# Performance work log

Measured on AMD Instinct MI355X. Metric: run time of the kernel, lower is better.

Reference implementation:

```python
import jax, jax.numpy as jnp
import numpy as np

B, C, F, T, D = 8, 128, 256, 128, 32


def setup_inputs() -> dict:
    key = jax.random.key(0)
    ks = jax.random.split(key, 7)
    x = jax.random.normal(ks[0], (B, C, F, T), jnp.float32)
    # 1x1 Conv2d over the T axis == linear map on T; weights [out, T], bias [out]
    Wk = jax.random.normal(ks[1], (D, T), jnp.float32) * 0.05
    bk = jax.random.normal(ks[2], (D,), jnp.float32) * 0.05
    Wq = jax.random.normal(ks[3], (D, T), jnp.float32) * 0.05
    bq = jax.random.normal(ks[4], (D,), jnp.float32) * 0.05
    Wv = jax.random.normal(ks[5], (T, T), jnp.float32) * 0.05
    bv = jax.random.normal(ks[6], (T,), jnp.float32) * 0.05
    return {"x": x, "Wk": Wk, "bk": bk, "Wq": Wq, "bq": bq, "Wv": Wv, "bv": bv}


def _proj(xp, W, b):
    # xp: [B, C2, F, T]; W: [out, T] -> [B, F, out, C2]
    return jnp.einsum('bcft,dt->bfdc', xp, W) + b[None, None, :, None]


def reference(x, Wk, bk, Wq, bq, Wv, bv):
    C2 = x.shape[1] // 2
    xr, xi = x[:, :C2], x[:, C2:]
    k_r = _proj(xr, Wk, bk)  # [B,F,D,C2]
    k_i = _proj(xi, Wk, bk)
    q_r = _proj(xr, Wq, bq)
    q_i = _proj(xi, Wq, bq)
    v_r = _proj(xr, Wv, bv)  # [B,F,T,C2]
    v_i = _proj(xi, Wv, bv)
    # complex P = k^H... actually plain k^T q (no conjugate in source)
    P_r = jnp.einsum('bfdc,bfde->bfce', k_r, q_r) - jnp.einsum('bfdc,bfde->bfce', k_i, q_i)
    P_i = jnp.einsum('bfdc,bfde->bfce', k_r, q_i) + jnp.einsum('bfdc,bfde->bfce', k_i, q_r)
    # independent softmaxes over dim=2 (the first C2 axis)
    W_r = jax.nn.softmax(P_r, axis=2)
    W_i = jax.nn.softmax(P_i, axis=2)
    # output = v @ W (complex)
    o_r = jnp.einsum('bftc,bfce->bfte', v_r, W_r) - jnp.einsum('bftc,bfce->bfte', v_i, W_i)
    o_i = jnp.einsum('bftc,bfce->bfte', v_r, W_i) + jnp.einsum('bftc,bfce->bfte', v_i, W_r)
    # permute [B,F,T,C2] -> [B,C2,F,T], concat real/imag on channel axis
    o_r = jnp.transpose(o_r, (0, 3, 1, 2))
    o_i = jnp.transpose(o_i, (0, 3, 1, 2))
    return jnp.concatenate([o_r, o_i], axis=1)  # [B,C,F,T]
```

## Files before the change

kernel.cpp:

```cpp
#include <hip/hip_runtime.h>

typedef __attribute__((ext_vector_type(8))) __bf16 bf16x8;
typedef __attribute__((ext_vector_type(8))) unsigned short ushort8;
typedef __attribute__((ext_vector_type(4))) unsigned short ushort4v;
typedef __attribute__((ext_vector_type(4))) float f32x4;

namespace {
constexpr int kB = 8, kC = 128, kF = 256, kT = 128;

__device__ __forceinline__ int addrXT(int t, int c) { return t * 128 + (c ^ ((t & 7) << 3)); }
__device__ __forceinline__ int addrU(int ri, int e, int s) { return ri * 8192 + e * 128 + (s ^ ((e & 7) << 3)); }
__device__ __forceinline__ int addrK(int mat, int c, int d) { return 16384 + mat * 2048 + c * 32 + (d ^ ((c & 3) << 3)); }
__device__ __forceinline__ int addrW(int ri, int e, int c) { return 16384 + ri * 4096 + e * 64 + (c ^ ((e & 7) << 3)); }

__device__ __forceinline__ unsigned short b16(float f) {
    __bf16 h = (__bf16)f;
    return __builtin_bit_cast(unsigned short, h);
}

__device__ __forceinline__ bf16x8 ldfrag(const unsigned short* lds, int idx) {
    return __builtin_bit_cast(bf16x8, *(const ushort8*)(lds + idx));
}

__device__ __forceinline__ bf16x8 fneg(bf16x8 a) {
    ushort8 u = __builtin_bit_cast(ushort8, a);
    u ^= (unsigned short)0x8000;
    return __builtin_bit_cast(bf16x8, u);
}

__device__ __forceinline__ bf16x8 fragWg(const float* p) {
    f32x4 a = *(const f32x4*)p;
    f32x4 c = *(const f32x4*)(p + 4);
    bf16x8 r;
    r[0] = (__bf16)a[0]; r[1] = (__bf16)a[1]; r[2] = (__bf16)a[2]; r[3] = (__bf16)a[3];
    r[4] = (__bf16)c[0]; r[5] = (__bf16)c[1]; r[6] = (__bf16)c[2]; r[7] = (__bf16)c[3];
    return r;
}
}

__global__ __launch_bounds__(256, 3)
void chanattn_mfma(const float* __restrict__ x,
                   const float* __restrict__ Wk, const float* __restrict__ bk,
                   const float* __restrict__ Wq, const float* __restrict__ bq,
                   const float* __restrict__ Wv, const float* __restrict__ bv,
                   float* __restrict__ out)
{
    __shared__ __align__(16) unsigned short lds[24576];

    const int f = blockIdx.x, b = blockIdx.y;
    const int tid = threadIdx.x;
    const int lane = tid & 63;
    const int w = tid >> 6;
    const int lr = lane & 15;
    const int lg = lane >> 4;
    const size_t cstr = (size_t)kF * kT;
    const float* xb = x + ((size_t)b * kC * kF + f) * kT;

    {
        const int tcol = tid & 15;
        const int rrow = tid >> 4;
        #pragma unroll
        for (int p = 0; p < 8; ++p) {
            const int r = 16 * p + rrow;
            const float* src = xb + (size_t)r * cstr;
            float v[8];
            #pragma unroll
            for (int q = 0; q < 8; ++q) v[q] = src[tcol + 16 * q];
            #pragma unroll
            for (int q = 0; q < 8; ++q) lds[addrXT(tcol + 16 * q, r)] = b16(v[q]);
        }
    }
    __syncthreads();

    {
        const float* Wm = (w < 2) ? Wk : Wq;
        const float* bm = (w < 2) ? bk : bq;
        const int crow0 = (w & 1) * 64;
        bf16x8 bw[2][4];
        #pragma unroll
        for (int dt = 0; dt < 2; ++dt)
            #pragma unroll
            for (int ks = 0; ks < 4; ++ks)
                bw[dt][ks] = fragWg(Wm + (size_t)(dt * 16 + lr) * kT + ks * 32 + 8 * lg);
        const float bias0 = bm[lr], bias1 = bm[16 + lr];

        #pragma unroll
        for (int ct = 0; ct < 4; ++ct) {
            f32x4 acc0 = {0.f, 0.f, 0.f, 0.f}, acc1 = {0.f, 0.f, 0.f, 0.f};
            #pragma unroll
            for (int ks = 0; ks < 4; ++ks) {
                bf16x8 a = fragWg(xb + (size_t)(crow0 + ct * 16 + lr) * cstr + ks * 32 + 8 * lg);
                acc0 = __builtin_amdgcn_mfma_f32_16x16x32_bf16(a, bw[0][ks], acc0, 0, 0, 0);
                acc1 = __builtin_amdgcn_mfma_f32_16x16x32_bf16(a, bw[1][ks], acc1, 0, 0, 0);
            }
            #pragma unroll
            for (int r = 0; r < 4; ++r) {
                const int c = ct * 16 + 4 * lg + r;
                lds[addrK(w, c, lr)]      = b16(acc0[r] + bias0);
                lds[addrK(w, c, 16 + lr)] = b16(acc1[r] + bias1);
            }
        }
    }
    __syncthreads();

    f32x4 pr[4], pi[4];
    float inv_r, inv_i;
    {
        const f32x4 zero = {0.f, 0.f, 0.f, 0.f};
        bf16x8 bqr = ldfrag(lds, addrK(2, 16 * w + lr, 8 * lg));
        bf16x8 bqi = ldfrag(lds, addrK(3, 16 * w + lr, 8 * lg));
        #pragma unroll
        for (int ct = 0; ct < 4; ++ct) {
            bf16x8 akr = ldfrag(lds, addrK(0, ct * 16 + lr, 8 * lg));
            bf16x8 aki = ldfrag(lds, addrK(1, ct * 16 + lr, 8 * lg));
            pr[ct] = __builtin_amdgcn_mfma_f32_16x16x32_bf16(akr, bqr, zero, 0, 0, 0);
            pr[ct] = __builtin_amdgcn_mfma_f32_16x16x32_bf16(fneg(aki), bqi, pr[ct], 0, 0, 0);
            pi[ct] = __builtin_amdgcn_mfma_f32_16x16x32_bf16(akr, bqi, zero, 0, 0, 0);
            pi[ct] = __builtin_amdgcn_mfma_f32_16x16x32_bf16(aki, bqr, pi[ct], 0, 0, 0);
        }
        float mr = -1e30f, mi = -1e30f;
        #pragma unroll
        for (int ct = 0; ct < 4; ++ct)
            #pragma unroll
            for (int r = 0; r < 4; ++r) { mr = fmaxf(mr, pr[ct][r]); mi = fmaxf(mi, pi[ct][r]); }
        mr = fmaxf(mr, __shfl_xor(mr, 16)); mr = fmaxf(mr, __shfl_xor(mr, 32));
        mi = fmaxf(mi, __shfl_xor(mi, 16)); mi = fmaxf(mi, __shfl_xor(mi, 32));
        float sr = 0.f, si = 0.f;
        #pragma unroll
        for (int ct = 0; ct < 4; ++ct)
            #pragma unroll
            for (int r = 0; r < 4; ++r) {
                float er = __expf(pr[ct][r] - mr); pr[ct][r] = er; sr += er;
                float ei = __expf(pi[ct][r] - mi); pi[ct][r] = ei; si += ei;
            }
        sr += __shfl_xor(sr, 16); sr += __shfl_xor(sr, 32);
        si += __shfl_xor(si, 16); si += __shfl_xor(si, 32);
        inv_r = 1.f / sr; inv_i = 1.f / si;
    }
    __syncthreads();
    {
        const int e = 16 * w + lr;
        #pragma unroll
        for (int ct = 0; ct < 4; ++ct) {
            ushort4v wr4, wi4;
            #pragma unroll
            for (int r = 0; r < 4; ++r) {
                wr4[r] = b16(pr[ct][r] * inv_r);
                wi4[r] = b16(pi[ct][r] * inv_i);
            }
            *(ushort4v*)&lds[addrW(0, e, ct * 16 + 4 * lg)] = wr4;
            *(ushort4v*)&lds[addrW(1, e, ct * 16 + 4 * lg)] = wi4;
        }
    }
    __syncthreads();

    f32x4 uacc_r[8], uacc_i[8];
    {
        bf16x8 awr[2], awi[2], awin[2];
        #pragma unroll
        for (int ks = 0; ks < 2; ++ks) {
            awr[ks]  = ldfrag(lds, addrW(0, 16 * w + lr, ks * 32 + 8 * lg));
            awi[ks]  = ldfrag(lds, addrW(1, 16 * w + lr, ks * 32 + 8 * lg));
            awin[ks] = fneg(awi[ks]);
        }
        #pragma unroll
        for (int nt = 0; nt < 8; ++nt) {
            f32x4 ur = {0.f, 0.f, 0.f, 0.f}, ui = {0.f, 0.f, 0.f, 0.f};
            #pragma unroll
            for (int ks = 0; ks < 2; ++ks) {
                bf16x8 bxr = ldfrag(lds, addrXT(nt * 16 + lr, ks * 32 + 8 * lg));
                bf16x8 bxi = ldfrag(lds, addrXT(nt * 16 + lr, 64 + ks * 32 + 8 * lg));
                ur = __builtin_amdgcn_mfma_f32_16x16x32_bf16(awr[ks], bxr, ur, 0, 0, 0);
                ur = __builtin_amdgcn_mfma_f32_16x16x32_bf16(awin[ks], bxi, ur, 0, 0, 0);
                ui = __builtin_amdgcn_mfma_f32_16x16x32_bf16(awi[ks], bxr, ui, 0, 0, 0);
                ui = __builtin_amdgcn_mfma_f32_16x16x32_bf16(awr[ks], bxi, ui, 0, 0, 0);
            }
            uacc_r[nt] = ur; uacc_i[nt] = ui;
        }
    }
    __syncthreads();
    {
        #pragma unroll
        for (int nt = 0; nt < 8; ++nt)
            #pragma unroll
            for (int r = 0; r < 4; ++r) {
                const int e = 16 * w + 4 * lg + r;
                lds[addrU(0, e, nt * 16 + lr)] = b16(uacc_r[nt][r]);
                lds[addrU(1, e, nt * 16 + lr)] = b16(uacc_i[nt][r]);
            }
    }
    __syncthreads();

    {
        #pragma unroll
        for (int mi_ = 0; mi_ < 2; ++mi_) {
            const int mt = 2 * w + mi_;
            bf16x8 av[4];
            #pragma unroll
            for (int ks = 0; ks < 4; ++ks)
                av[ks] = fragWg(Wv + (size_t)(mt * 16 + lr) * kT + ks * 32 + 8 * lg);
            float bvv[4];
            #pragma unroll
            for (int r = 0; r < 4; ++r) bvv[r] = 2.f * bv[mt * 16 + 4 * lg + r];

            #pragma unroll
            for (int et = 0; et < 4; ++et) {
                f32x4 aor = {0.f, 0.f, 0.f, 0.f}, aoi = {0.f, 0.f, 0.f, 0.f};
                #pragma unroll
                for (int ks = 0; ks < 4; ++ks) {
                    bf16x8 bur = ldfrag(lds, addrU(0, et * 16 + lr, ks * 32 + 8 * lg));
                    bf16x8 bui = ldfrag(lds, addrU(1, et * 16 + lr, ks * 32 + 8 * lg));
                    aor = __builtin_amdgcn_mfma_f32_16x16x32_bf16(av[ks], bur, aor, 0, 0, 0);
                    aoi = __builtin_amdgcn_mfma_f32_16x16x32_bf16(av[ks], bui, aoi, 0, 0, 0);
                }
                const int e = et * 16 + lr;
                const int tp0 = mt * 16 + 4 * lg;
                f32x4 vi;
                #pragma unroll
                for (int r = 0; r < 4; ++r) vi[r] = aoi[r] + bvv[r];
                *(f32x4*)(out + (((size_t)b * kC + e) * kF + f) * kT + tp0)      = aor;
                *(f32x4*)(out + (((size_t)b * kC + 64 + e) * kF + f) * kT + tp0) = vi;
            }
        }
    }
}

extern "C" void kernel_launch(void* const* d_in, const int* in_sizes, int n_in,
                              void* d_out, int out_size, void* d_ws, size_t ws_size,
                              hipStream_t stream) {
    const float* x  = (const float*)d_in[0];
    const float* Wk = (const float*)d_in[1];
    const float* bk = (const float*)d_in[2];
    const float* Wq = (const float*)d_in[3];
    const float* bq = (const float*)d_in[4];
    const float* Wv = (const float*)d_in[5];
    const float* bv = (const float*)d_in[6];
    float* out = (float*)d_out;

    dim3 grid(kF, kB);
    dim3 block(256);
    chanattn_mfma<<<grid, block, 0, stream>>>(x, Wk, bk, Wq, bq, Wv, bv, out);
}
```

Before: 93.47 us.

## Keep Q and softmax weights in registers, permute channels to cut LDS round-trips

Each wave now computes its own Q projection in an MFMA layout that feeds the P=K^T Q product straight from registers. It also turns the softmax output directly into A-operand fragments, which removes the LDS staging of Q and W and two barriers. The x tile is written to LDS with a permuted channel order so the K layout matches the register fragments, and loads use vectorised float4 reads. LDS use drops and the launch bound goes from 3 to 4 blocks per CU, which raises occupancy but tightens register pressure.

```diff
diff --git a/kernel.cpp b/kernel.cpp
--- a/kernel.cpp
+++ b/kernel.cpp
@@ -8,10 +8,9 @@
 namespace {
 constexpr int kB = 8, kC = 128, kF = 256, kT = 128;
 
-__device__ __forceinline__ int addrXT(int t, int c) { return t * 128 + (c ^ ((t & 7) << 3)); }
+__device__ __forceinline__ int addrXT(int t, int p) { return t * 128 + (p ^ ((t & 7) << 3)); }
 __device__ __forceinline__ int addrU(int ri, int e, int s) { return ri * 8192 + e * 128 + (s ^ ((e & 7) << 3)); }
-__device__ __forceinline__ int addrK(int mat, int c, int d) { return 16384 + mat * 2048 + c * 32 + (d ^ ((c & 3) << 3)); }
-__device__ __forceinline__ int addrW(int ri, int e, int c) { return 16384 + ri * 4096 + e * 64 + (c ^ ((e & 7) << 3)); }
+__device__ __forceinline__ int addrK(int m, int c, int p) { return 16384 + m * 2048 + c * 32 + (p ^ ((c & 3) << 3)); }
 
 __device__ __forceinline__ unsigned short b16(float f) {
     __bf16 h = (__bf16)f;
@@ -38,14 +37,14 @@
 }
 }
 
-__global__ __launch_bounds__(256, 3)
-void chanattn_mfma(const float* __restrict__ x,
-                   const float* __restrict__ Wk, const float* __restrict__ bk,
-                   const float* __restrict__ Wq, const float* __restrict__ bq,
-                   const float* __restrict__ Wv, const float* __restrict__ bv,
-                   float* __restrict__ out)
+__global__ __launch_bounds__(256, 4)
+void chanattn_mfma2(const float* __restrict__ x,
+                    const float* __restrict__ Wk, const float* __restrict__ bk,
+                    const float* __restrict__ Wq, const float* __restrict__ bq,
+                    const float* __restrict__ Wv, const float* __restrict__ bv,
+                    float* __restrict__ out)
 {
-    __shared__ __align__(16) unsigned short lds[24576];
+    __shared__ __align__(16) unsigned short lds[20480];
 
     const int f = blockIdx.x, b = blockIdx.y;
     const int tid = threadIdx.x;
@@ -56,48 +55,73 @@
     const size_t cstr = (size_t)kF * kT;
     const float* xb = x + ((size_t)b * kC * kF + f) * kT;
 
-    {
-        const int tcol = tid & 15;
-        const int rrow = tid >> 4;
-        #pragma unroll
-        for (int p = 0; p < 8; ++p) {
-            const int r = 16 * p + rrow;
-            const float* src = xb + (size_t)r * cstr;
-            float v[8];
-            #pragma unroll
-            for (int q = 0; q < 8; ++q) v[q] = src[tcol + 16 * q];
-            #pragma unroll
-            for (int q = 0; q < 8; ++q) lds[addrXT(tcol + 16 * q, r)] = b16(v[q]);
-        }
-    }
-    __syncthreads();
-
-    {
-        const float* Wm = (w < 2) ? Wk : Wq;
-        const float* bm = (w < 2) ? bk : bq;
-        const int crow0 = (w & 1) * 64;
-        bf16x8 bw[2][4];
+    bf16x8 bqr, bqi;
+    {
+        bf16x8 xr_f[4], xi_f[4];
+        #pragma unroll
+        for (int ks = 0; ks < 4; ++ks) {
+            xr_f[ks] = fragWg(xb + (size_t)(16 * w + lr) * cstr + ks * 32 + 8 * lg);
+            xi_f[ks] = fragWg(xb + (size_t)(64 + 16 * w + lr) * cstr + ks * 32 + 8 * lg);
+        }
+        f32x4 qacc[2][2], kacc[2][2];
+        #pragma unroll
+        for (int ri = 0; ri < 2; ++ri)
+            #pragma unroll
+            for (int dt = 0; dt < 2; ++dt) {
+                qacc[ri][dt] = (f32x4){0.f, 0.f, 0.f, 0.f};
+                kacc[ri][dt] = (f32x4){0.f, 0.f, 0.f, 0.f};
+            }
         #pragma unroll
         for (int dt = 0; dt < 2; ++dt)
             #pragma unroll
-            for (int ks = 0; ks < 4; ++ks)
-                bw[dt][ks] = fragWg(Wm + (size_t)(dt * 16 + lr) * kT + ks * 32 + 8 * lg);
-        const float bias0 = bm[lr], bias1 = bm[16 + lr];
-
-        #pragma unroll
-        for (int ct = 0; ct < 4; ++ct) {
-            f32x4 acc0 = {0.f, 0.f, 0.f, 0.f}, acc1 = {0.f, 0.f, 0.f, 0.f};
-            #pragma unroll
             for (int ks = 0; ks < 4; ++ks) {
-                bf16x8 a = fragWg(xb + (size_t)(crow0 + ct * 16 + lr) * cstr + ks * 32 + 8 * lg);
-                acc0 = __builtin_amdgcn_mfma_f32_16x16x32_bf16(a, bw[0][ks], acc0, 0, 0, 0);
-                acc1 = __builtin_amdgcn_mfma_f32_16x16x32_bf16(a, bw[1][ks], acc1, 0, 0, 0);
-            }
+                bf16x8 wq = fragWg(Wq + (size_t)(16 * dt + lr) * kT + ks * 32 + 8 * lg);
+                bf16x8 wk = fragWg(Wk + (size_t)(16 * dt + lr) * kT + ks * 32 + 8 * lg);
+                qacc[0][dt] = __builtin_amdgcn_mfma_f32_16x16x32_bf16(wq, xr_f[ks], qacc[0][dt], 0, 0, 0);
+                qacc[1][dt] = __builtin_amdgcn_mfma_f32_16x16x32_bf16(wq, xi_f[ks], qacc[1][dt], 0, 0, 0);
+                kacc[0][dt] = __builtin_amdgcn_mfma_f32_16x16x32_bf16(xr_f[ks], wk, kacc[0][dt], 0, 0, 0);
+                kacc[1][dt] = __builtin_amdgcn_mfma_f32_16x16x32_bf16(xi_f[ks], wk, kacc[1][dt], 0, 0, 0);
+            }
+        const float bk0 = bk[lr], bk1 = bk[16 + lr];
+        #pragma unroll
+        for (int dt = 0; dt < 2; ++dt) {
+            const int pcol = 8 * ((lr >> 2) & 3) + 4 * dt + (lr & 3);
+            const float bb = dt ? bk1 : bk0;
             #pragma unroll
             for (int r = 0; r < 4; ++r) {
-                const int c = ct * 16 + 4 * lg + r;
-                lds[addrK(w, c, lr)]      = b16(acc0[r] + bias0);
-                lds[addrK(w, c, 16 + lr)] = b16(acc1[r] + bias1);
+                const int c = 16 * w + 4 * lg + r;
+                lds[addrK(0, c, pcol)] = b16(kacc[0][dt][r] + bb);
+                lds[addrK(1, c, pcol)] = b16(kacc[1][dt][r] + bb);
+            }
+        }
+        #pragma unroll
+        for (int j = 0; j < 8; ++j) {
+            const int dt = j >> 2, r = j & 3;
+            const float bb = bq[16 * dt + 4 * lg + r];
+            bqr[j] = (__bf16)(qacc[0][dt][r] + bb);
+            bqi[j] = (__bf16)(qacc[1][dt][r] + bb);
+        }
+    }
+
+    {
+        const int c0 = 4 * (tid & 31);
+        const int t0 = 4 * (tid >> 5);
+        const int h  = c0 >> 6;
+        const int cc = c0 & 63;
+        const int p0 = 64 * h + 32 * (cc >> 5) + 8 * ((cc >> 2) & 3) + 4 * ((cc >> 4) & 1);
+        #pragma unroll
+        for (int tp = 0; tp < 4; ++tp) {
+            const int t = t0 + 32 * tp;
+            f32x4 v[4];
+            #pragma unroll
+            for (int j = 0; j < 4; ++j)
+                v[j] = *(const f32x4*)(xb + (size_t)(c0 + j) * cstr + t);
+            #pragma unroll
+            for (int i = 0; i < 4; ++i) {
+                ushort4v pk;
+                pk[0] = b16(v[0][i]); pk[1] = b16(v[1][i]);
+                pk[2] = b16(v[2][i]); pk[3] = b16(v[3][i]);
+                *(ushort4v*)&lds[addrXT(t + i, p0)] = pk;
             }
         }
     }
@@ -107,8 +131,6 @@
     float inv_r, inv_i;
     {
         const f32x4 zero = {0.f, 0.f, 0.f, 0.f};
-        bf16x8 bqr = ldfrag(lds, addrK(2, 16 * w + lr, 8 * lg));
-        bf16x8 bqi = ldfrag(lds, addrK(3, 16 * w + lr, 8 * lg));
         #pragma unroll
         for (int ct = 0; ct < 4; ++ct) {
             bf16x8 akr = ldfrag(lds, addrK(0, ct * 16 + lr, 8 * lg));
@@ -137,58 +159,43 @@
         si += __shfl_xor(si, 16); si += __shfl_xor(si, 32);
         inv_r = 1.f / sr; inv_i = 1.f / si;
     }
+
+    bf16x8 awr[2], awi[2], awin[2];
+    #pragma unroll
+    for (int ks = 0; ks < 2; ++ks) {
+        #pragma unroll
+        for (int j = 0; j < 8; ++j) {
+            const int ct = 2 * ks + (j >> 2), r = j & 3;
+            awr[ks][j] = (__bf16)(pr[ct][r] * inv_r);
+            awi[ks][j] = (__bf16)(pi[ct][r] * inv_i);
+        }
+        awin[ks] = fneg(awi[ks]);
+    }
+
+    f32x4 uacc_r[8], uacc_i[8];
+    #pragma unroll
+    for (int nt = 0; nt < 8; ++nt) {
+        f32x4 ur = {0.f, 0.f, 0.f, 0.f}, ui = {0.f, 0.f, 0.f, 0.f};
+        #pragma unroll
+        for (int ks = 0; ks < 2; ++ks) {
+            bf16x8 bxr = ldfrag(lds, addrXT(nt * 16 + lr, ks * 32 + 8 * lg));
+            bf16x8 bxi = ldfrag(lds, addrXT(nt * 16 + lr, 64 + ks * 32 + 8 * lg));
+            ur = __builtin_amdgcn_mfma_f32_16x16x32_bf16(awr[ks], bxr, ur, 0, 0, 0);
+            ur = __builtin_amdgcn_mfma_f32_16x16x32_bf16(awin[ks], bxi, ur, 0, 0, 0);
+            ui = __builtin_amdgcn_mfma_f32_16x16x32_bf16(awi[ks], bxr, ui, 0, 0, 0);
+            ui = __builtin_amdgcn_mfma_f32_16x16x32_bf16(awr[ks], bxi, ui, 0, 0, 0);
+        }
+        uacc_r[nt] = ur; uacc_i[nt] = ui;
+    }
     __syncthreads();
-    {
-        const int e = 16 * w + lr;
-        #pragma unroll
-        for (int ct = 0; ct < 4; ++ct) {
-            ushort4v wr4, wi4;
-            #pragma unroll
-            for (int r = 0; r < 4; ++r) {
-                wr4[r] = b16(pr[ct][r] * inv_r);
-                wi4[r] = b16(pi[ct][r] * inv_i);
-            }
-            *(ushort4v*)&lds[addrW(0, e, ct * 16 + 4 * lg)] = wr4;
-            *(ushort4v*)&lds[addrW(1, e, ct * 16 + 4 * lg)] = wi4;
-        }
-    }
-    __syncthreads();
-
-    f32x4 uacc_r[8], uacc_i[8];
-    {
-        bf16x8 awr[2], awi[2], awin[2];
-        #pragma unroll
-        for (int ks = 0; ks < 2; ++ks) {
-            awr[ks]  = ldfrag(lds, addrW(0, 16 * w + lr, ks * 32 + 8 * lg));
-            awi[ks]  = ldfrag(lds, addrW(1, 16 * w + lr, ks * 32 + 8 * lg));
-            awin[ks] = fneg(awi[ks]);
-        }
-        #pragma unroll
-        for (int nt = 0; nt < 8; ++nt) {
-            f32x4 ur = {0.f, 0.f, 0.f, 0.f}, ui = {0.f, 0.f, 0.f, 0.f};
-            #pragma unroll
-            for (int ks = 0; ks < 2; ++ks) {
-                bf16x8 bxr = ldfrag(lds, addrXT(nt * 16 + lr, ks * 32 + 8 * lg));
-                bf16x8 bxi = ldfrag(lds, addrXT(nt * 16 + lr, 64 + ks * 32 + 8 * lg));
-                ur = __builtin_amdgcn_mfma_f32_16x16x32_bf16(awr[ks], bxr, ur, 0, 0, 0);
-                ur = __builtin_amdgcn_mfma_f32_16x16x32_bf16(awin[ks], bxi, ur, 0, 0, 0);
-                ui = __builtin_amdgcn_mfma_f32_16x16x32_bf16(awi[ks], bxr, ui, 0, 0, 0);
-                ui = __builtin_amdgcn_mfma_f32_16x16x32_bf16(awr[ks], bxi, ui, 0, 0, 0);
-            }
-            uacc_r[nt] = ur; uacc_i[nt] = ui;
-        }
-    }
-    __syncthreads();
-    {
-        #pragma unroll
-        for (int nt = 0; nt < 8; ++nt)
-            #pragma unroll
-            for (int r = 0; r < 4; ++r) {
-                const int e = 16 * w + 4 * lg + r;
-                lds[addrU(0, e, nt * 16 + lr)] = b16(uacc_r[nt][r]);
-                lds[addrU(1, e, nt * 16 + lr)] = b16(uacc_i[nt][r]);
-            }
-    }
+    #pragma unroll
+    for (int nt = 0; nt < 8; ++nt)
+        #pragma unroll
+        for (int r = 0; r < 4; ++r) {
+            const int e = 16 * w + 4 * lg + r;
+            lds[addrU(0, e, nt * 16 + lr)] = b16(uacc_r[nt][r]);
+            lds[addrU(1, e, nt * 16 + lr)] = b16(uacc_i[nt][r]);
+        }
     __syncthreads();
 
     {
@@ -239,5 +246,5 @@
 
     dim3 grid(kF, kB);
     dim3 block(256);
-    chanattn_mfma<<<grid, block, 0, stream>>>(x, Wk, bk, Wq, bq, Wv, bv, out);
-}
+    chanattn_mfma2<<<grid, block, 0, stream>>>(x, Wk, bk, Wq, bq, Wv, bv, out);
+}
```

Result: slower. 97.59 us (+4.4%).
